# Performance work log

Measured on AMD Instinct MI355X. Metric: run time of the kernel, lower is better.

## Reference

```python
import jax, jax.numpy as jnp
import numpy as np

# ---------------- irreps metadata: list of (mul, l, parity) ----------------
IR_A  = [(1, 0, 1)]                                        # '0e' input scalars
IR_B  = [(10,0,1),(10,0,-1),(10,0,1),(5,1,1),(5,1,-1)]     # Gate input, dim 60
IR_C  = [(10,0,1),(10,0,-1),(5,1,1),(5,1,-1)]              # Gate output, dim 50
IR_D  = [(1,0,-1),(6,0,1)]                                 # '0o + 6x0e', dim 7
IR_SH = [(1,0,1),(1,1,-1)]                                 # '0e + 1o'
CONVS = [(IR_A,IR_B),(IR_C,IR_B),(IR_C,IR_B),(IR_C,IR_B),(IR_C,IR_D)]
R_BASIS  = 2
DIAMETER = 5.0   # source used 1.5 -> degenerate 1^3 kernel; enlarged to exercise the steerable conv
STEP     = 1.0

def irdim(ir):
    return sum(m*(2*l+1) for m,l,_ in ir)

def irslices(ir):
    out, o = [], 0
    for m,l,_ in ir:
        d = m*(2*l+1); out.append(slice(o,o+d)); o += d
    return out

# normalized Clebsch-Gordan (wigner3j * sqrt(2*l_out+1)) for l<=1
_eps = np.zeros((3,3,3))
for a,b,c in [(0,1,2),(1,2,0),(2,0,1)]:
    _eps[a,b,c] = 1.0; _eps[b,a,c] = -1.0
CG = {
    (0,0,0): np.ones((1,1,1)),
    (0,1,1): np.eye(3).reshape(1,3,3),
    (1,0,1): np.eye(3).reshape(3,1,3),
    (1,1,0): (np.eye(3)/np.sqrt(3.0)).reshape(3,3,1),
    (1,1,1): _eps/np.sqrt(2.0),
}

def tp_ins(ir1, iro):
    ins = []
    for i1,(m1,l1,p1) in enumerate(ir1):
        for i2,(m2,l2,p2) in enumerate(IR_SH):
            for io,(mo,lo,po) in enumerate(iro):
                if po == p1*p2 and abs(l1-l2) <= lo <= l1+l2:
                    ins.append((i1,i2,io))
    return ins

def tp_numel(ir1, iro):
    return sum(R_BASIS*ir1[i1][0]*IR_SH[i2][0]*iro[io][0] for i1,i2,io in tp_ins(ir1,iro))

def lin_ins(ir1, iro):
    return [(i,j) for i,(m1,l1,p1) in enumerate(ir1)
                  for j,(m2,l2,p2) in enumerate(iro) if l1==l2 and p1==p2]

def lin_numel(ir1, iro):
    return sum(ir1[i][0]*iro[j][0] for i,j in lin_ins(ir1,iro))

def _lattice_features():
    # lattice offsets, smooth_finite radial basis (with cutoff) and SH ('0e+1o', component norm)
    r = DIAMETER/2.0
    s = int(np.floor(r/STEP))
    c = np.arange(-s, s+1, dtype=np.float64)*STEP
    lat = np.stack(np.meshgrid(c, c, c, indexing='ij'), -1)            # [K,K,K,3]
    d = np.linalg.norm(lat, axis=-1)
    vals = np.linspace(0.0, r, R_BASIS+2)[1:-1]
    step = vals[1]-vals[0]
    diff = (d[...,None]-vals)/step
    sus = lambda t: np.where(t>0, np.exp(-1.0/np.where(t>0, t, 1.0)), 0.0)
    emb = 1.14136*np.exp(2.0)*sus(diff+1.0)*sus(1.0-diff)              # [K,K,K,R]
    unit = lat/np.maximum(d, 1e-9)[...,None]
    sh = np.concatenate([np.ones_like(d)[...,None],
                         np.sqrt(3.0)*unit[...,[1,2,0]]], -1)          # [K,K,K,4], e3nn (y,z,x) order
    return jnp.asarray(emb, jnp.float32), jnp.asarray(sh, jnp.float32)

EMB, SH = _lattice_features()

def build_kernel(ir_in, ir_out, tw, lw):
    sin, sout, ssh = irslices(ir_in), irslices(ir_out), irslices(IR_SH)
    K = EMB.shape[0]
    k = jnp.zeros((K, K, K, irdim(ir_in), irdim(ir_out)), jnp.float32)
    off = 0
    for i1,i2,io in tp_ins(ir_in, ir_out):
        m1,l1,_ = ir_in[i1]; m2,l2,_ = IR_SH[i2]; mo,lo,_ = ir_out[io]
        n = R_BASIS*m1*m2*mo
        w = tw[off:off+n].reshape(R_BASIS, m1, mo); off += n           # m2 == 1 for SH
        cg = jnp.asarray(CG[(l1,l2,lo)], jnp.float32)
        alpha = 1.0/np.sqrt(m1*m2*R_BASIS)
        shseg = SH[..., ssh[i2]]                                       # [K,K,K,2l2+1]
        blk = alpha*jnp.einsum('xyzr,ruw,xyzj,ijk->xyzuiwk', EMB, w, shseg, cg)
        k = k.at[:,:,:, sin[i1], sout[io]].add(
            blk.reshape(K, K, K, m1*(2*l1+1), mo*(2*lo+1)))
    # self-connection Linear at the kernel center (radial basis vanishes at r=0)
    M = jnp.zeros((irdim(ir_in), irdim(ir_out)), jnp.float32)
    off = 0
    for i,j in lin_ins(ir_in, ir_out):
        m1,l1,_ = ir_in[i]; mo,_,_ = ir_out[j]
        w = lw[off:off+m1*mo].reshape(m1, mo); off += m1*mo
        eye = jnp.eye(2*l1+1, dtype=jnp.float32)
        blk = (1.0/np.sqrt(m1))*jnp.einsum('uw,ik->uiwk', w, eye)
        M = M.at[sin[i], sout[j]].add(blk.reshape(m1*(2*l1+1), mo*(2*l1+1)))
    cc = K//2
    return k.at[cc, cc, cc].set(M)

def equiv_conv(x, k):
    return jax.lax.conv_general_dilated(x, k, (1,1,1), 'SAME',
        dimension_numbers=('NXYZC', 'XYZIO', 'NXYZC'))

def gate(y):
    # Gate('10x0e+10x0o', [gelu, tanh], '10x0e', [sigmoid], '5x1e+5x1o')
    s = jnp.concatenate([jax.nn.gelu(y[..., :10]), jnp.tanh(y[..., 10:20])], -1)
    g = jax.nn.sigmoid(y[..., 20:30])                                  # 10 gate scalars
    v = y[..., 30:60].reshape(y.shape[:-1]+(10,3))*g[..., None]        # gate 5x1e + 5x1o
    return jnp.concatenate([s, v.reshape(y.shape[:-1]+(30,))], -1)

def _forward(x, tws, lws):
    y = x
    for i,(a,b) in enumerate(CONVS):
        y = equiv_conv(y, build_kernel(a, b, tws[i], lws[i]))
        if i < len(CONVS)-1:
            y = gate(y)
    return jnp.sum(y, axis=(1, 2, 3))                                  # [B, 7]

def setup_inputs() -> dict:
    key = jax.random.key(0)
    ks = jax.random.split(key, 11)
    inp = {'x': jax.random.normal(ks[0], (2, 48, 48, 48, 1), jnp.float32)}
    for i,(a,b) in enumerate(CONVS):
        inp[f'tp_w{i}'] = jax.random.normal(ks[1+i], (tp_numel(a,b),), jnp.float32)
        inp[f'lin_w{i}'] = jax.random.normal(ks[6+i], (lin_numel(a,b),), jnp.float32)
    return inp

def reference(x, tp_w0, tp_w1, tp_w2, tp_w3, tp_w4,
              lin_w0, lin_w1, lin_w2, lin_w3, lin_w4):
    return _forward(x, [tp_w0, tp_w1, tp_w2, tp_w3, tp_w4],
                    [lin_w0, lin_w1, lin_w2, lin_w3, lin_w4])
```

## Files before the change

kernel.cpp:

```cpp
#include <hip/hip_runtime.h>
#include <hip/hip_bf16.h>
#include <math.h>


typedef __attribute__((ext_vector_type(8))) short bf16x8;
typedef __attribute__((ext_vector_type(4))) float f32x4;
typedef __attribute__((ext_vector_type(4))) unsigned int u32x4;

struct TpPath { int off, ci, co, m1, l1, i2, mo, lo; float alpha; };
struct LinPath { int off, ci, co, m1, l, mo; float norm; };

__device__ __constant__ TpPath g_tp[19] = {
  {0,  0,  0, 1, 0, 0, 10, 0, 0.70710678f},
  {20, 0, 20, 1, 0, 0, 10, 0, 0.70710678f},
  {40, 0, 45, 1, 0, 1,  5, 1, 0.70710678f},
  {0,    0,  0, 10, 0, 0, 10, 0, 0.22360680f},
  {200,  0, 20, 10, 0, 0, 10, 0, 0.22360680f},
  {400,  0, 45, 10, 0, 1,  5, 1, 0.22360680f},
  {500, 10, 10, 10, 0, 0, 10, 0, 0.22360680f},
  {700, 10, 30, 10, 0, 1,  5, 1, 0.22360680f},
  {800, 20, 30,  5, 1, 0,  5, 1, 0.31622777f},
  {850, 20, 10,  5, 1, 1, 10, 0, 0.31622777f},
  {950, 20, 45,  5, 1, 1,  5, 1, 0.31622777f},
  {1000,35, 45,  5, 1, 0,  5, 1, 0.31622777f},
  {1050,35,  0,  5, 1, 1, 10, 0, 0.31622777f},
  {1150,35, 20,  5, 1, 1, 10, 0, 0.31622777f},
  {1250,35, 30,  5, 1, 1,  5, 1, 0.31622777f},
  {0,    0, 1, 10, 0, 0, 6, 0, 0.22360680f},
  {120, 10, 0, 10, 0, 0, 1, 0, 0.22360680f},
  {140, 20, 0,  5, 1, 1, 1, 0, 0.31622777f},
  {150, 35, 1,  5, 1, 1, 6, 0, 0.31622777f},
};

__device__ __constant__ LinPath g_lin[9] = {
  {0,  0,  0, 1, 0, 10, 1.0f},
  {10, 0, 20, 1, 0, 10, 1.0f},
  {0,   0,  0, 10, 0, 10, 0.31622777f},
  {100, 0, 20, 10, 0, 10, 0.31622777f},
  {200,10, 10, 10, 0, 10, 0.31622777f},
  {300,20, 30,  5, 1,  5, 0.44721360f},
  {325,35, 45,  5, 1,  5, 0.44721360f},
  {0,  0, 1, 10, 0, 6, 0.31622777f},
  {60,10, 0, 10, 0, 1, 0.31622777f},
};

__device__ inline float sus_f(float t) { return t > 0.f ? __expf(-1.f / t) : 0.f; }

__global__ void build_tp_kernel(const float* __restrict__ tw, float* __restrict__ kbuf,
                                int CIN, int COUT, int path_base) {
  TpPath p = g_tp[path_base + blockIdx.x];
  const int dl1 = 2 * p.l1 + 1, dlo = 2 * p.lo + 1;
  const int du = p.m1 * dl1, dw = p.mo * dlo;
  const int total = 125 * du * dw;
  const float C0 = 1.14136f * expf(2.0f);
  for (int e = threadIdx.x; e < total; e += blockDim.x) {
    int xyz = e / (du * dw);
    int rem = e % (du * dw);
    int ui = rem / dw, wk = rem % dw;
    int u = ui / dl1, i = ui % dl1;
    int w = wk / dlo, kk = wk % dlo;
    int kx = xyz / 25, ky = (xyz / 5) % 5, kz = xyz % 5;
    float cx = (float)(kx - 2), cy = (float)(ky - 2), cz = (float)(kz - 2);
    float d = sqrtf(cx * cx + cy * cy + cz * cz);
    float t = 1.2f * d;
    float e0 = C0 * sus_f(t) * sus_f(2.f - t);
    float e1 = C0 * sus_f(t - 1.f) * sus_f(3.f - t);
    float radial = e0 * tw[p.off + (0 * p.m1 + u) * p.mo + w] +
                   e1 * tw[p.off + (1 * p.m1 + u) * p.mo + w];
    float invd = (d > 0.f) ? 1.f / d : 0.f;
    const float s3 = 1.7320508f;
    float sh1[3] = { s3 * cy * invd, s3 * cz * invd, s3 * cx * invd };
    float shfac;
    if (p.l1 == 0 && p.i2 == 0)      shfac = 1.f;
    else if (p.l1 == 0)              shfac = sh1[kk];
    else if (p.i2 == 0)              shfac = (i == kk) ? 1.f : 0.f;
    else if (p.lo == 0)              shfac = sh1[i] * 0.57735027f;
    else {
      if (i == kk) shfac = 0.f;
      else {
        int j = 3 - i - kk;
        float sgn = (j == (i + 1) % 3) ? 1.f : -1.f;
        shfac = sgn * sh1[j] * 0.70710678f;
      }
    }
    kbuf[(size_t)(xyz * CIN + p.ci + ui) * COUT + p.co + wk] = p.alpha * radial * shfac;
  }
}

__global__ void set_center_kernel(const float* __restrict__ lw, float* __restrict__ kbuf,
                                  int CIN, int COUT, int lin_base, int nlin) {
  for (int l = 0; l < nlin; l++) {
    LinPath q = g_lin[lin_base + l];
    int dl = 2 * q.l + 1;
    int tot = q.m1 * q.mo * dl;
    for (int e = threadIdx.x; e < tot; e += blockDim.x) {
      int u = e / (q.mo * dl);
      int r = e % (q.mo * dl);
      int w = r / dl, ii = r % dl;
      kbuf[(size_t)(62 * CIN + q.ci + u * dl + ii) * COUT + q.co + w * dl + ii] =
          q.norm * lw[q.off + u * q.mo + w];
    }
  }
}

__global__ void convert_w(const float* __restrict__ kbuf, unsigned short* __restrict__ kwbT,
                          int CIN, int COUT) {
  int idx = blockIdx.x * 256 + threadIdx.x;
  if (idx >= 125 * 64 * 64) return;
  int tap = idx >> 12, co = (idx >> 6) & 63, ci = idx & 63;
  float v = (ci < CIN && co < COUT) ? kbuf[((size_t)tap * CIN + ci) * COUT + co] : 0.f;
  __hip_bfloat16 h = __float2bfloat16(v);
  kwbT[idx] = *(unsigned short*)&h;
}

__global__ void build_w0(const float* __restrict__ k0, unsigned short* __restrict__ wb0L) {
  int idx = blockIdx.x * 256 + threadIdx.x;
  if (idx >= 5 * 2 * 64 * 32) return;
  int k = idx & 31, co = (idx >> 5) & 63, mf = (idx >> 11) & 1, dxi = idx >> 12;
  float v = 0.f;
  if (co < 60) {
    if (mf == 0) {
      int dy = k >> 3, dz = k & 7;
      if (dz < 5) v = k0[(size_t)(((dxi * 5 + dy) * 5 + dz)) * 60 + co];
    } else {
      int kg = k >> 3, dz = k & 7;
      if (kg == 0 && dz < 5) v = k0[(size_t)(((dxi * 5 + 4) * 5 + dz)) * 60 + co];
    }
  }
  __hip_bfloat16 h = __float2bfloat16(v);
  wb0L[idx] = *(unsigned short*)&h;
}

__device__ inline float gelu_f(float x) {
  float inner = 0.79788456f * (x + 0.044715f * x * x * x);
  return 0.5f * x * (1.f + tanhf(inner));
}
__device__ inline float sigm_f(float x) { return 1.f / (1.f + __expf(-x)); }

__device__ inline int eidx(int c, int z) {
  return c * 16 + ((((z >> 2) ^ (c & 3)) << 2) | (z & 3));
}
__device__ inline int oidx(int z, int p) { return z * 32 + (p ^ z); }
__device__ inline int uidx(int e) {
  return (e & ~31) | ((e & 31) ^ ((e >> 5) & 15));
}

__device__ inline void gate_tile(const float* my, unsigned int* myO, int z) {
#pragma unroll
  for (int p = 0; p < 25; p++) {
    float a0, a1;
    if (p < 5) {
      a0 = gelu_f(my[eidx(2 * p, z)]);
      a1 = gelu_f(my[eidx(2 * p + 1, z)]);
    } else if (p < 10) {
      a0 = tanhf(my[eidx(2 * p, z)]);
      a1 = tanhf(my[eidx(2 * p + 1, z)]);
    } else {
      int q0 = 2 * (p - 10), q1 = q0 + 1;
      a0 = my[eidx(30 + q0, z)] * sigm_f(my[eidx(20 + q0 / 3, z)]);
      a1 = my[eidx(30 + q1, z)] * sigm_f(my[eidx(20 + q1 / 3, z)]);
    }
    __hip_bfloat162 p2;
    p2.x = __float2bfloat16(a0);
    p2.y = __float2bfloat16(a1);
    myO[oidx(z, p)] = *(unsigned int*)&p2;
  }
#pragma unroll
  for (int p = 25; p < 32; p++) myO[oidx(z, p)] = 0u;
}

template <int NT>
__device__ inline void epilogue_gate(f32x4 (&acc)[3][NT], float* my,
                                     unsigned short* out_, int n, int x, int y,
                                     int l, int lm, int kg) {
  unsigned int* myO = (unsigned int*)(my + 1024);
#pragma unroll
  for (int zt = 0; zt < 3; zt++) {
#pragma unroll
    for (int nt = 0; nt < NT; nt++)
      *(f32x4*)(my + (lm + 16 * nt) * 16 + ((kg ^ (lm & 3)) << 2)) = acc[zt][nt];
    if (l < 16) gate_tile(my, myO, l);
    unsigned int* gout = (unsigned int*)out_ +
        ((size_t)(((n * 48 + x) * 48 + y) * 48 + 16 * zt)) * 32;
#pragma unroll 1
    for (int e = l; e < 512; e += 64) gout[e] = myO[uidx(e)];
  }
}

template <int CIN, int COUT, int MODE>
__global__ __launch_bounds__(768, 3)
void conv_mfma(const unsigned short* __restrict__ act, const short* __restrict__ kwbT,
               const unsigned short* __restrict__ zguard, void* __restrict__ out_) {
  constexpr int NTH = (MODE == 0) ? 2 : 1;
  constexpr int KC = (CIN + 31) / 32;
  __shared__ __align__(16) unsigned int Albs[16 * 48 * 32];

  const int tid = threadIdx.x;
  const int l = tid & 63;
  const int w = tid >> 6;
  const int wp = (MODE == 0) ? (w % 6) : w;
  const int ch = (MODE == 0) ? (w / 6) : 0;
  const int lm = l & 15;
  const int kg = l >> 4;
  const int co_off = ch * 32;

  const int bid = blockIdx.x;
  const int yb = bid % 4;
  const int x = (bid / 4) % 48;
  const int n = bid / (4 * 48);

  int g_off[8]; bool g_ok[8];
#pragma unroll
  for (int i = 0; i < 8; i++) {
    int e = tid + i * 768;
    int yi = e / 384;
    int rem = e % 384;
    int zin = rem >> 3, u = rem & 7;
    int usrc = u ^ (zin & 7);
    int yin = 12 * yb + yi - 2;
    g_ok[i] = (yin >= 0) && (yin < 48);
    int yc = min(max(yin, 0), 47);
    g_off[i] = (yc * 48 + zin) * 64 + usrc * 8;
  }

  f32x4 acc[2][3][NTH];
#pragma unroll
  for (int yy = 0; yy < 2; yy++)
#pragma unroll
    for (int zt = 0; zt < 3; zt++)
#pragma unroll
      for (int nt = 0; nt < NTH; nt++) acc[yy][zt][nt] = (f32x4){0.f, 0.f, 0.f, 0.f};

  const int xlo = max(x - 2, 0), xhi = min(x + 2, 47);

#pragma unroll 1
  for (int xin = xlo; xin <= xhi; ++xin) {
    __syncthreads();
    const unsigned short* pb = act + (size_t)((n * 48 + xin) * 2304) * 64;
#pragma unroll
    for (int i = 0; i < 8; i++) {
      const unsigned short* src = g_ok[i] ? (pb + g_off[i]) : zguard;
      __builtin_amdgcn_global_load_lds(
          (const __attribute__((address_space(1))) unsigned int*)src,
          (__attribute__((address_space(3))) unsigned int*)(Albs + (size_t)(i * 768 + w * 64) * 4),
          16, 0, 0);
    }
    __syncthreads();

    if (MODE == 0 || w < 6) {
      const int dxi = xin - x + 2;
      const short* Albs_s = (const short*)Albs;
#pragma unroll 1
      for (int dy = 0; dy < 5; dy++) {
        const int tapbase = (dxi * 5 + dy) * 5;
#pragma unroll
        for (int dz = 0; dz < 5; dz++) {
          bf16x8 bfr[NTH * KC];
          {
            const short* wb_ = kwbT + ((size_t)(tapbase + dz) << 12) +
                               (co_off + lm) * 64 + kg * 8;
#pragma unroll
            for (int nt = 0; nt < NTH; nt++)
#pragma unroll
              for (int kc = 0; kc < KC; kc++)
                bfr[nt * KC + kc] = *(const bf16x8*)(wb_ + nt * 1024 + kc * 32);
          }
          bf16x8 afr[2][3][KC];
#pragma unroll
          for (int zt = 0; zt < 3; zt++) {
            const int zraw = 16 * zt + lm + dz - 2;
            const int zc = min(max(zraw, 0), 47);
            const bool zval = (zraw >= 0) && (zraw < 48);
#pragma unroll
            for (int yy = 0; yy < 2; yy++) {
              const int yrow = 2 * wp + yy + dy;
              const int rowoff = (yrow * 48 + zc) * 64;
#pragma unroll
              for (int kc = 0; kc < KC; kc++) {
                int u = (4 * kc + kg) ^ (zc & 7);
                bf16x8 v = *(const bf16x8*)(Albs_s + rowoff + u * 8);
                afr[yy][zt][kc] = zval ? v : (bf16x8)(short)0;
              }
            }
          }
#pragma unroll
          for (int yy = 0; yy < 2; yy++)
#pragma unroll
            for (int zt = 0; zt < 3; zt++)
#pragma unroll
              for (int nt = 0; nt < NTH; nt++)
#pragma unroll
                for (int kc = 0; kc < KC; kc++)
                  acc[yy][zt][nt] = __builtin_amdgcn_mfma_f32_16x16x32_bf16(
                      afr[yy][zt][kc], bfr[nt * KC + kc], acc[yy][zt][nt], 0, 0, 0);
        }
      }
    }
  }

  if constexpr (MODE == 0) {
    __syncthreads();
    float* base = (float*)Albs;
    int par = 0;
#pragma unroll
    for (int yy = 0; yy < 2; yy++) {
#pragma unroll
      for (int zt = 0; zt < 3; zt++) {
        float* my = base + par * 9216 + wp * 1536;
        unsigned int* myO = (unsigned int*)(my + 1024);
#pragma unroll
        for (int nt = 0; nt < NTH; nt++)
          *(f32x4*)(my + (co_off + lm + 16 * nt) * 16 + ((kg ^ (lm & 3)) << 2)) =
              acc[yy][zt][nt];
        __syncthreads();
        if (ch == 0 && l < 16) gate_tile(my, myO, l);
        __syncthreads();
        unsigned int* gout = (unsigned int*)out_ +
            ((size_t)(((n * 48 + x) * 48 + (12 * yb + 2 * wp + yy)) * 48 + 16 * zt)) * 32;
#pragma unroll
        for (int q = 0; q < 4; q++) {
          int e = ch * 256 + q * 64 + l;
          gout[e] = myO[uidx(e)];
        }
        par ^= 1;
      }
    }
  } else {
    if (w < 6) {
      float s = 0.f;
#pragma unroll
      for (int yy = 0; yy < 2; yy++)
#pragma unroll
        for (int zt = 0; zt < 3; zt++)
#pragma unroll
          for (int r = 0; r < 4; r++) s += acc[yy][zt][0][r];
      s += __shfl_xor(s, 16);
      s += __shfl_xor(s, 32);
      if (l < 7) atomicAdd(&((float*)out_)[n * 7 + l], s);
    }
  }
}

__global__ __launch_bounds__(256, 4)
void conv0_mfma(const float* __restrict__ in_, const short* __restrict__ wb0L,
                unsigned short* __restrict__ out_) {
  __shared__ float A0[8 * 72];
  __shared__ __align__(16) float outbuf0[4 * 1536];

  const int tid = threadIdx.x;
  const int l = tid & 63;
  const int w = tid >> 6;
  const int lm = l & 15;
  const int kg = l >> 4;
  const int yb = blockIdx.x % 12;
  const int x = (blockIdx.x / 12) % 48;
  const int n = blockIdx.x / (12 * 48);

  f32x4 acc[3][4];
#pragma unroll
  for (int zt = 0; zt < 3; zt++)
#pragma unroll
    for (int nt = 0; nt < 4; nt++) acc[zt][nt] = (f32x4){0.f, 0.f, 0.f, 0.f};

  for (int dxi = 0; dxi < 5; dxi++) {
    int xin = x + dxi - 2;
    if (xin < 0 || xin >= 48) continue;
    __syncthreads();
    for (int e = tid; e < 8 * 72; e += 256) {
      int yi = e / 72, zz = e % 72;
      int yin = 4 * yb + yi - 2, zin = zz - 2;
      A0[e] = (yin >= 0 && yin < 48 && zin >= 0 && zin < 48)
                  ? in_[(size_t)((n * 48 + xin) * 48 + yin) * 48 + zin] : 0.f;
    }
    __syncthreads();
#pragma unroll
    for (int mf = 0; mf < 2; mf++) {
      const short* wbp = wb0L + ((size_t)(dxi * 2 + mf) * 64 + lm) * 32 + kg * 8;
      bf16x8 bfr[4];
#pragma unroll
      for (int nt = 0; nt < 4; nt++) bfr[nt] = *(const bf16x8*)(wbp + nt * 16 * 32);
      const int row = mf ? (w + 4) : (w + kg);
#pragma unroll
      for (int zt = 0; zt < 3; zt++) {
        const float* ap = A0 + row * 72 + 16 * zt + lm;
        union { bf16x8 v; unsigned short s[8]; } af;
#pragma unroll
        for (int j = 0; j < 8; j++) {
          __hip_bfloat16 h = __float2bfloat16(ap[j]);
          af.s[j] = *(unsigned short*)&h;
        }
#pragma unroll
        for (int nt = 0; nt < 4; nt++)
          acc[zt][nt] = __builtin_amdgcn_mfma_f32_16x16x32_bf16(
              af.v, bfr[nt], acc[zt][nt], 0, 0, 0);
      }
    }
  }

  float* my = outbuf0 + w * 1536;
  epilogue_gate<4>(acc, my, out_, n, x, 4 * yb + w, l, lm, kg);
}

extern "C" void kernel_launch(void* const* d_in, const int* in_sizes, int n_in,
                              void* d_out, int out_size, void* d_ws, size_t ws_size,
                              hipStream_t stream) {
  const float* x   = (const float*)d_in[0];
  const float* tw0 = (const float*)d_in[1];
  const float* lw0 = (const float*)d_in[2];
  const float* tw1 = (const float*)d_in[3];
  const float* lw1 = (const float*)d_in[4];
  const float* tw2 = (const float*)d_in[5];
  const float* lw2 = (const float*)d_in[6];
  const float* tw3 = (const float*)d_in[7];
  const float* lw3 = (const float*)d_in[8];
  const float* tw4 = (const float*)d_in[9];
  const float* lw4 = (const float*)d_in[10];

  float* ws = (float*)d_ws;
  float* k0 = ws;
  float* k1 = k0 + 7500;
  float* k2 = k1 + 375000;
  float* k3 = k2 + 375000;
  float* k4 = k3 + 375000;
  unsigned short* actA = (unsigned short*)(ws + 1200000);
  unsigned short* actB = actA + 14155776;
  unsigned short* wb1 = (unsigned short*)(ws + 15360000);
  unsigned short* wb2 = wb1 + 512000;
  unsigned short* wb3 = wb2 + 512000;
  unsigned short* wb4 = wb3 + 512000;
  unsigned short* wb0L = wb4 + 512000;
  unsigned short* zg   = wb0L + 20480;

  hipMemsetAsync(ws, 0, (size_t)1176250 * sizeof(float), stream);
  hipMemsetAsync(zg, 0, 64, stream);
  hipMemsetAsync(d_out, 0, (size_t)out_size * sizeof(float), stream);

  build_tp_kernel<<<3, 128, 0, stream>>>(tw0, k0, 1, 60, 0);
  build_tp_kernel<<<12, 128, 0, stream>>>(tw1, k1, 50, 60, 3);
  build_tp_kernel<<<12, 128, 0, stream>>>(tw2, k2, 50, 60, 3);
  build_tp_kernel<<<12, 128, 0, stream>>>(tw3, k3, 50, 60, 3);
  build_tp_kernel<<<4, 128, 0, stream>>>(tw4, k4, 50, 7, 15);
  set_center_kernel<<<1, 256, 0, stream>>>(lw0, k0, 1, 60, 0, 2);
  set_center_kernel<<<1, 256, 0, stream>>>(lw1, k1, 50, 60, 2, 5);
  set_center_kernel<<<1, 256, 0, stream>>>(lw2, k2, 50, 60, 2, 5);
  set_center_kernel<<<1, 256, 0, stream>>>(lw3, k3, 50, 60, 2, 5);
  set_center_kernel<<<1, 256, 0, stream>>>(lw4, k4, 50, 7, 7, 2);

  convert_w<<<2000, 256, 0, stream>>>(k1, wb1, 50, 60);
  convert_w<<<2000, 256, 0, stream>>>(k2, wb2, 50, 60);
  convert_w<<<2000, 256, 0, stream>>>(k3, wb3, 50, 60);
  convert_w<<<2000, 256, 0, stream>>>(k4, wb4, 50, 7);
  build_w0<<<80, 256, 0, stream>>>(k0, wb0L);

  const int grid0 = 2 * 48 * 12;
  const int grid  = 2 * 48 * 4;
  conv0_mfma<<<grid0, 256, 0, stream>>>(x, (const short*)wb0L, actA);
  conv_mfma<50, 60, 0><<<grid, 768, 0, stream>>>(actA, (const short*)wb1, zg, actB);
  conv_mfma<50, 60, 0><<<grid, 768, 0, stream>>>(actB, (const short*)wb2, zg, actA);
  conv_mfma<50, 60, 0><<<grid, 768, 0, stream>>>(actA, (const short*)wb3, zg, actB);
  conv_mfma<50, 7, 1><<<grid, 768, 0, stream>>>(actB, (const short*)wb4, zg, d_out);
}
```

Baseline: 1.930 ms.

## Replace final conv with separable box-sum reduction and small contraction

Because the last layer's output is summed over all spatial positions, the final convolution is linear and can be reduced to per-tap windowed sums of the input activations. Separable z/y/x prefix-style sums compute, for each kernel offset, the sum of input channels over the valid shifted region; a tiny kernel then contracts these with the fp32 kernel weights. This removes a full MFMA convolution pass over the volume and its bf16 weight conversion, adding several small reduction kernels, including a serial single-block x pass. It also reuses workspace buffers (actA, k1, k2) as scratch for the intermediate sums.

```diff
diff --git a/kernel.cpp b/kernel.cpp
--- a/kernel.cpp
+++ b/kernel.cpp
@@ -401,6 +401,92 @@
   epilogue_gate<4>(acc, my, out_, n, x, 4 * yb + w, l, lm, kg);
 }
 
+__global__ void sum_z(const unsigned short* __restrict__ act, float* __restrict__ zs) {
+  int gw = blockIdx.x * 4 + (threadIdx.x >> 6);
+  int ci = threadIdx.x & 63;
+  const unsigned short* p = act + (size_t)gw * 48 * 64 + ci;
+  float tot = 0.f, s0 = 0.f, s1 = 0.f, s46 = 0.f, s47 = 0.f;
+#pragma unroll 4
+  for (int z = 0; z < 48; z++) {
+    unsigned short h = p[z * 64];
+    float v = __bfloat162float(*(__hip_bfloat16*)&h);
+    tot += v;
+    if (z == 0) s0 = v;
+    if (z == 1) s1 = v;
+    if (z == 46) s46 = v;
+    if (z == 47) s47 = v;
+  }
+  float* o = zs + (size_t)gw * 320 + ci;
+  o[0]   = tot - s46 - s47;
+  o[64]  = tot - s47;
+  o[128] = tot;
+  o[192] = tot - s0;
+  o[256] = tot - s0 - s1;
+}
+
+__global__ void sum_y(const float* __restrict__ zs, float* __restrict__ ys) {
+  int gw = blockIdx.x * 4 + (threadIdx.x >> 6);
+  int ci = threadIdx.x & 63;
+#pragma unroll 1
+  for (int rz = 0; rz < 5; rz++) {
+    const float* p = zs + (size_t)gw * 48 * 320 + rz * 64 + ci;
+    float tot = 0.f, s0 = 0.f, s1 = 0.f, s46 = 0.f, s47 = 0.f;
+    for (int y = 0; y < 48; y++) {
+      float v = p[y * 320];
+      tot += v;
+      if (y == 0) s0 = v;
+      if (y == 1) s1 = v;
+      if (y == 46) s46 = v;
+      if (y == 47) s47 = v;
+    }
+    float* o = ys + (size_t)gw * 1600 + rz * 64 + ci;
+    o[0]    = tot - s46 - s47;
+    o[320]  = tot - s47;
+    o[640]  = tot;
+    o[960]  = tot - s0;
+    o[1280] = tot - s0 - s1;
+  }
+}
+
+__global__ void sum_x(const float* __restrict__ ys, float* __restrict__ xs) {
+  int n = threadIdx.x >> 6;
+  int ci = threadIdx.x & 63;
+#pragma unroll 1
+  for (int ry = 0; ry < 5; ry++)
+    for (int rz = 0; rz < 5; rz++) {
+      const float* p = ys + (size_t)(n * 48) * 1600 + ry * 320 + rz * 64 + ci;
+      float tot = 0.f, s0 = 0.f, s1 = 0.f, s46 = 0.f, s47 = 0.f;
+      for (int xx = 0; xx < 48; xx++) {
+        float v = p[(size_t)xx * 1600];
+        tot += v;
+        if (xx == 0) s0 = v;
+        if (xx == 1) s1 = v;
+        if (xx == 46) s46 = v;
+        if (xx == 47) s47 = v;
+      }
+      float* o = xs + (size_t)n * 8000 + (ry * 5 + rz) * 64 + ci;
+      o[0]    = tot - s46 - s47;
+      o[1600] = tot - s47;
+      o[3200] = tot;
+      o[4800] = tot - s0;
+      o[6400] = tot - s0 - s1;
+    }
+}
+
+__global__ void contract4(const float* __restrict__ k4, const float* __restrict__ xs,
+                          float* __restrict__ out) {
+  int t = threadIdx.x;
+  int pair = t & 15, chunk = t >> 4;
+  if (pair >= 14) return;
+  int n = pair / 7, co = pair % 7;
+  int t0 = chunk * 8, t1 = min(t0 + 8, 125);
+  float s = 0.f;
+  for (int tap = t0; tap < t1; tap++)
+    for (int ci = 0; ci < 50; ci++)
+      s += k4[((size_t)tap * 50 + ci) * 7 + co] * xs[(size_t)n * 8000 + tap * 64 + ci];
+  atomicAdd(&out[n * 7 + co], s);
+}
+
 extern "C" void kernel_launch(void* const* d_in, const int* in_sizes, int n_in,
                               void* d_out, int out_size, void* d_ws, size_t ws_size,
                               hipStream_t stream) {
@@ -427,9 +513,11 @@
   unsigned short* wb1 = (unsigned short*)(ws + 15360000);
   unsigned short* wb2 = wb1 + 512000;
   unsigned short* wb3 = wb2 + 512000;
-  unsigned short* wb4 = wb3 + 512000;
-  unsigned short* wb0L = wb4 + 512000;
+  unsigned short* wb0L = wb3 + 512000;
   unsigned short* zg   = wb0L + 20480;
+  float* zs = (float*)actA;
+  float* ys = k1;
+  float* xs = k2;
 
   hipMemsetAsync(ws, 0, (size_t)1176250 * sizeof(float), stream);
   hipMemsetAsync(zg, 0, 64, stream);
@@ -449,7 +537,6 @@
   convert_w<<<2000, 256, 0, stream>>>(k1, wb1, 50, 60);
   convert_w<<<2000, 256, 0, stream>>>(k2, wb2, 50, 60);
   convert_w<<<2000, 256, 0, stream>>>(k3, wb3, 50, 60);
-  convert_w<<<2000, 256, 0, stream>>>(k4, wb4, 50, 7);
   build_w0<<<80, 256, 0, stream>>>(k0, wb0L);
 
   const int grid0 = 2 * 48 * 12;
@@ -458,5 +545,8 @@
   conv_mfma<50, 60, 0><<<grid, 768, 0, stream>>>(actA, (const short*)wb1, zg, actB);
   conv_mfma<50, 60, 0><<<grid, 768, 0, stream>>>(actB, (const short*)wb2, zg, actA);
   conv_mfma<50, 60, 0><<<grid, 768, 0, stream>>>(actA, (const short*)wb3, zg, actB);
-  conv_mfma<50, 7, 1><<<grid, 768, 0, stream>>>(actB, (const short*)wb4, zg, d_out);
-}
+  sum_z<<<1152, 256, 0, stream>>>(actB, zs);
+  sum_y<<<24, 256, 0, stream>>>(zs, ys);
+  sum_x<<<1, 128, 0, stream>>>(ys, xs);
+  contract4<<<1, 256, 0, stream>>>(k4, xs, (float*)d_out);
+}
```

New measurement: 1.938 ms. About the same (+0.5%).
